# Kernel optimization log

Measured on AMD Instinct MI355X. Metric: run time of the kernel, lower is better.

Reference implementation:

```python
import jax, jax.numpy as jnp
import numpy as np
from jax import lax

B, T, D, H, O, L = 128, 2048, 64, 128, 32, 2


def _rnn_layer(x, lengths, W_ih, W_hh, b_ih, b_hh):
    """One tanh RNN layer over padded [B,T,*] input with packed semantics:
    hidden state is frozen at steps t >= lengths[b] (those steps do not exist
    in the packed sequence). Returns per-step hidden states [B,T,H]."""
    Bl, Tl, _ = x.shape
    Hl = W_hh.shape[0]
    # precompute input projection once: [B,T,H]
    x_proj = jnp.einsum('btd,hd->bth', x, W_ih) + b_ih + b_hh

    def step(h, inp):
        xp, t = inp  # xp: [B,H], t: scalar
        h_new = jnp.tanh(xp + h @ W_hh.T)
        h = jnp.where((t < lengths)[:, None], h_new, h)
        return h, h

    h0 = jnp.zeros((Bl, Hl), dtype=x.dtype)
    _, ys = lax.scan(step, h0, (x_proj.transpose(1, 0, 2), jnp.arange(Tl)))
    return ys.transpose(1, 0, 2)  # [B,T,H]


def setup_inputs() -> dict:
    key = jax.random.key(0)
    ks = jax.random.split(key, 12)
    x = jax.random.normal(ks[0], (B, T, D), dtype=jnp.float32)
    # descending-sorted lengths in [1, T] (pack_padded_sequence enforce_sorted)
    lengths = jnp.sort(jax.random.randint(ks[1], (B,), 1, T + 1).astype(jnp.int32))[::-1]
    s_in = 1.0 / np.sqrt(H)
    W_ih0 = jax.random.uniform(ks[2], (H, D), minval=-s_in, maxval=s_in)
    W_hh0 = jax.random.uniform(ks[3], (H, H), minval=-s_in, maxval=s_in)
    b_ih0 = jax.random.uniform(ks[4], (H,), minval=-s_in, maxval=s_in)
    b_hh0 = jax.random.uniform(ks[5], (H,), minval=-s_in, maxval=s_in)
    W_ih1 = jax.random.uniform(ks[6], (H, H), minval=-s_in, maxval=s_in)
    W_hh1 = jax.random.uniform(ks[7], (H, H), minval=-s_in, maxval=s_in)
    b_ih1 = jax.random.uniform(ks[8], (H,), minval=-s_in, maxval=s_in)
    b_hh1 = jax.random.uniform(ks[9], (H,), minval=-s_in, maxval=s_in)
    W_fc = jax.random.uniform(ks[10], (O, H), minval=-s_in, maxval=s_in)
    b_fc = jax.random.uniform(ks[11], (O,), minval=-s_in, maxval=s_in)
    return {"x": x, "lengths": lengths,
            "W_ih0": W_ih0, "W_hh0": W_hh0, "b_ih0": b_ih0, "b_hh0": b_hh0,
            "W_ih1": W_ih1, "W_hh1": W_hh1, "b_ih1": b_ih1, "b_hh1": b_hh1,
            "W_fc": W_fc, "b_fc": b_fc}


def reference(x, lengths, W_ih0, W_hh0, b_ih0, b_hh0,
              W_ih1, W_hh1, b_ih1, b_hh1, W_fc, b_fc):
    h1 = _rnn_layer(x, lengths, W_ih0, W_hh0, b_ih0, b_hh0)   # [B,T,H]
    h2 = _rnn_layer(h1, lengths, W_ih1, W_hh1, b_ih1, b_hh1)  # [B,T,H]
    # pad_packed_sequence zero-fills positions t >= length
    mask = (jnp.arange(T)[None, :] < lengths[:, None])[..., None]
    out = jnp.where(mask, h2, 0.0)
    # fc is applied to the zero-padded tensor (padded rows become b_fc)
    return jnp.einsum('bth,oh->bto', out, W_fc) + b_fc
```

## Files before the change

kernel.cpp:

```cpp
#include <hip/hip_runtime.h>

#define BB 128
#define TT 2048
#define DD 64
#define HH 128
#define OO 32

typedef _Float16 f16x8 __attribute__((ext_vector_type(8)));
typedef float    f32x4 __attribute__((ext_vector_type(4)));

#define MFMA16(a,b,c) __builtin_amdgcn_mfma_f32_16x16x32_f16((a),(b),(c),0,0,0)

__device__ __forceinline__ f32x4 load4(const float* p){ return *(const f32x4*)p; }

__device__ __forceinline__ f16x8 afrag(const float* p){
    float4 a = *(const float4*)p, b = *(const float4*)(p+4);
    f16x8 r;
    r[0]=(_Float16)a.x; r[1]=(_Float16)a.y; r[2]=(_Float16)a.z; r[3]=(_Float16)a.w;
    r[4]=(_Float16)b.x; r[5]=(_Float16)b.y; r[6]=(_Float16)b.z; r[7]=(_Float16)b.w;
    return r;
}

__device__ __forceinline__ float tanh5(float u){
#if __has_builtin(__builtin_amdgcn_exp2f)
    float e = __builtin_amdgcn_exp2f(u * 2.885390081777927f);
#else
    float e = exp2f(u * 2.885390081777927f);
#endif
    return __builtin_fmaf(-2.f, __builtin_amdgcn_rcpf(1.f + e), 1.f);
}

#define XSTR 72
extern "C" __global__ void __launch_bounds__(256)
proj_kernel(const float* __restrict__ x, const float* __restrict__ W_ih0,
            const float* __restrict__ b_ih0, const float* __restrict__ b_hh0,
            _Float16* __restrict__ xp0)
{
    const int tid = threadIdx.x;
    const int w = tid >> 6, lane = tid & 63;
    const int n = lane & 15, q = lane >> 4;
    const size_t row0 = (size_t)blockIdx.x * 64;

    __shared__ __align__(16) _Float16 XT[64][XSTR];

    #pragma unroll
    for (int it = 0; it < 4; ++it){
        float4 v = *(const float4*)(x + row0*DD + it*1024 + tid*4);
        int rr = it*16 + (tid >> 4), d0 = (tid & 15)*4;
        union { uint2 u; _Float16 h[4]; } c;
        c.h[0]=(_Float16)v.x; c.h[1]=(_Float16)v.y; c.h[2]=(_Float16)v.z; c.h[3]=(_Float16)v.w;
        *(uint2*)&XT[rr][d0] = c.u;
    }

    f16x8 A[8][2]; f32x4 bv[8];
    #pragma unroll
    for (int mt = 0; mt < 8; ++mt){
        #pragma unroll
        for (int kt = 0; kt < 2; ++kt)
            A[mt][kt] = afrag(W_ih0 + (mt*16 + n)*DD + kt*32 + q*8);
        bv[mt] = load4(b_ih0 + mt*16 + q*4) + load4(b_hh0 + mt*16 + q*4);
    }
    __syncthreads();

    const _Float16* xr = &XT[w*16 + n][0];
    f16x8 B0 = *(const f16x8*)(xr + q*8);
    f16x8 B1 = *(const f16x8*)(xr + 32 + q*8);

    _Float16* orow = xp0 + (row0 + w*16 + n)*HH + q*4;
    #pragma unroll
    for (int mt = 0; mt < 8; ++mt){
        f32x4 acc = bv[mt];
        acc = MFMA16(A[mt][0], B0, acc);
        acc = MFMA16(A[mt][1], B1, acc);
        union { uint2 u; _Float16 h[4]; } s;
        #pragma unroll
        for (int r = 0; r < 4; ++r) s.h[r] = (_Float16)acc[r];
        *(uint2*)(orow + mt*16) = s.u;
    }
}

extern "C" __global__ void __launch_bounds__(256)
fill_kernel(const int* __restrict__ lengths, const float* __restrict__ b_fc,
            float* __restrict__ out)
{
    size_t idx = (size_t)blockIdx.x*256 + threadIdx.x;
    #pragma unroll
    for (int k = 0; k < 4; ++k, idx += (size_t)2048*256){
        int o4 = (int)(idx & 7);
        int t  = (int)((idx >> 3) & 2047);
        int b  = (int)(idx >> 14);
        if (t >= lengths[b])
            ((float4*)out)[idx] = *(const float4*)(b_fc + o4*4);
    }
}

#define NB   16
#define LSTR 136

extern "C" __global__ void __launch_bounds__(256, 1)
scan_kernel(const _Float16* __restrict__ xp0, const int* __restrict__ lengths,
            const float* __restrict__ W_hh0,
            const float* __restrict__ W_ih1, const float* __restrict__ W_hh1,
            const float* __restrict__ b_ih1, const float* __restrict__ b_hh1,
            const float* __restrict__ W_fc,  const float* __restrict__ b_fc,
            float* __restrict__ out)
{
    const int tid  = threadIdx.x;
    const int w    = tid >> 6, lane = tid & 63;
    const int n    = lane & 15, q = lane >> 4;
    const int rbase= blockIdx.x * NB;

    __shared__ __align__(16) _Float16 H1T[2][NB][LSTR];
    __shared__ __align__(16) _Float16 H2T[2][NB][LSTR];

    for (int idx = tid; idx < 2*NB*LSTR/2; idx += 256){
        ((unsigned*)H1T)[idx] = 0u;
        ((unsigned*)H2T)[idx] = 0u;
    }

    f16x8 A0[2][4], Ai[2][4], Ah[2][4];
    #pragma unroll
    for (int m = 0; m < 2; ++m){
        const int row = (2*w + m)*16 + n;
        #pragma unroll
        for (int kt = 0; kt < 4; ++kt){
            A0[m][kt] = afrag(W_hh0 + row*HH + kt*32 + q*8);
            Ai[m][kt] = afrag(W_ih1 + row*HH + kt*32 + q*8);
            Ah[m][kt] = afrag(W_hh1 + row*HH + kt*32 + q*8);
        }
    }
    const int f = w & 1;
    f16x8 Af[4];
    #pragma unroll
    for (int kt = 0; kt < 4; ++kt)
        Af[kt] = afrag(W_fc + (f*16 + n)*HH + kt*32 + q*8);

    f32x4 b1v[2];
    #pragma unroll
    for (int m = 0; m < 2; ++m)
        b1v[m] = load4(b_ih1 + (2*w+m)*16 + q*4) + load4(b_hh1 + (2*w+m)*16 + q*4);
    const f32x4 bfv = load4(b_fc + f*16 + q*4);

    const int lenn = lengths[rbase + n];
    int mx = lenn;
    #pragma unroll
    for (int s = 1; s < 16; s <<= 1){ int o = __shfl_xor(mx, s, 64); mx = max(mx, o); }
    const int maxlen = __builtin_amdgcn_readfirstlane(mx);

    const _Float16* xpbase = xp0 + ((size_t)(rbase+n)*TT)*HH + (2*w)*16 + q*4;
    float* obase = out + ((size_t)(rbase+n)*TT)*OO + f*16 + q*4;

    uint2 xcA, xcB, xnA, xnB;
    xcA = *(const uint2*)(xpbase);            xcB = *(const uint2*)(xpbase + 16);
    if (1 < maxlen){ xnA = *(const uint2*)(xpbase + HH); xnB = *(const uint2*)(xpbase + HH + 16); }

    __syncthreads();

    for (int t = 0; t <= maxlen + 1; ++t){
        const int p = t & 1, pn = p ^ 1;

        f16x8 bh1[4], bh2[4];
        #pragma unroll
        for (int kt = 0; kt < 4; ++kt){
            bh1[kt] = *(const f16x8*)&H1T[p][n][kt*32 + q*8];
            bh2[kt] = *(const f16x8*)&H2T[p][n][kt*32 + q*8];
        }

        f32x4 z0[2];
        const bool doZ0 = (t < maxlen);
        if (doZ0){
            {
                union { uint2 u; _Float16 h[4]; } cA, cB; cA.u = xcA; cB.u = xcB;
                #pragma unroll
                for (int r = 0; r < 4; ++r){ z0[0][r] = (float)cA.h[r]; z0[1][r] = (float)cB.h[r]; }
            }
            if (t + 2 < maxlen){
                xcA = *(const uint2*)(xpbase + (size_t)(t+2)*HH);
                xcB = *(const uint2*)(xpbase + (size_t)(t+2)*HH + 16);
            }
            #pragma unroll
            for (int kt = 0; kt < 4; ++kt){
                z0[0] = MFMA16(A0[0][kt], bh1[kt], z0[0]);
                z0[1] = MFMA16(A0[1][kt], bh1[kt], z0[1]);
            }
        }

        f32x4 z1[2];
        const bool doZ1 = (t >= 1) && (t <= maxlen);
        if (doZ1){
            z1[0] = b1v[0]; z1[1] = b1v[1];
            #pragma unroll
            for (int kt = 0; kt < 4; ++kt){
                z1[0] = MFMA16(Ai[0][kt], bh1[kt], z1[0]);
                z1[1] = MFMA16(Ai[1][kt], bh1[kt], z1[1]);
            }
            #pragma unroll
            for (int kt = 0; kt < 4; ++kt){
                z1[0] = MFMA16(Ah[0][kt], bh2[kt], z1[0]);
                z1[1] = MFMA16(Ah[1][kt], bh2[kt], z1[1]);
            }
        }

        if (w >= 2 && t >= 2){
            f32x4 zf = bfv;
            #pragma unroll
            for (int kt = 0; kt < 4; ++kt) zf = MFMA16(Af[kt], bh2[kt], zf);
            if (t - 2 < lenn){
                float4 sv; sv.x = zf[0]; sv.y = zf[1]; sv.z = zf[2]; sv.w = zf[3];
                *(float4*)(obase + (size_t)(t-2)*OO) = sv;
            }
        }

        if (doZ0){
            #pragma unroll
            for (int m = 0; m < 2; ++m){
                union { uint2 u; _Float16 h[4]; } s;
                #pragma unroll
                for (int r = 0; r < 4; ++r) s.h[r] = (_Float16)tanh5(z0[m][r]);
                *(uint2*)&H1T[pn][n][(2*w+m)*16 + q*4] = s.u;
            }
        }
        if (doZ1){
            #pragma unroll
            for (int m = 0; m < 2; ++m){
                union { uint2 u; _Float16 h[4]; } s;
                #pragma unroll
                for (int r = 0; r < 4; ++r) s.h[r] = (_Float16)tanh5(z1[m][r]);
                *(uint2*)&H2T[pn][n][(2*w+m)*16 + q*4] = s.u;
            }
        }

        { uint2 tA = xcA; xcA = xnA; xnA = tA; uint2 tB = xcB; xcB = xnB; xnB = tB; }

        asm volatile("s_waitcnt lgkmcnt(0)\n\ts_barrier" ::: "memory");
    }
}

extern "C" void kernel_launch(void* const* d_in, const int* in_sizes, int n_in,
                              void* d_out, int out_size, void* d_ws, size_t ws_size,
                              hipStream_t stream)
{
    const float* x       = (const float*)d_in[0];
    const int*   lengths = (const int*)  d_in[1];
    const float* W_ih0   = (const float*)d_in[2];
    const float* W_hh0   = (const float*)d_in[3];
    const float* b_ih0   = (const float*)d_in[4];
    const float* b_hh0   = (const float*)d_in[5];
    const float* W_ih1   = (const float*)d_in[6];
    const float* W_hh1   = (const float*)d_in[7];
    const float* b_ih1   = (const float*)d_in[8];
    const float* b_hh1   = (const float*)d_in[9];
    const float* W_fc    = (const float*)d_in[10];
    const float* b_fc    = (const float*)d_in[11];

    _Float16* xp = (_Float16*)d_ws;

    proj_kernel<<<BB*TT/64, 256, 0, stream>>>(x, W_ih0, b_ih0, b_hh0, xp);
    fill_kernel<<<2048, 256, 0, stream>>>(lengths, b_fc, (float*)d_out);
    scan_kernel<<<BB/NB, 256, 0, stream>>>(xp, lengths, W_hh0,
                                           W_ih1, W_hh1, b_ih1, b_hh1,
                                           W_fc, b_fc, (float*)d_out);
}
```

Measured before the change: 1.783 ms.

## Pack two batch groups per workgroup with per-group LDS counter barriers

The scan kernel now launches 4 workgroups of 512 threads instead of 8 of 256. Each workgroup holds two independent 16-row batch groups, each with its own LDS state buffers. The per-step s_barrier is replaced by a per-group LDS atomic counter with a spin-wait, so the two groups synchronise independently. The intent is to cut barrier cost and let the two groups' waves interleave on one CU. In exchange it uses fewer CUs, adds atomic and spin-polling overhead, and doubles per-thread register pressure demands under the 512,2 launch bounds, which may force spills of the weight fragments.

```diff
diff --git a/kernel.cpp b/kernel.cpp
--- a/kernel.cpp
+++ b/kernel.cpp
@@ -97,7 +97,7 @@
 #define NB   16
 #define LSTR 136
 
-extern "C" __global__ void __launch_bounds__(256, 1)
+extern "C" __global__ void __launch_bounds__(512, 2)
 scan_kernel(const _Float16* __restrict__ xp0, const int* __restrict__ lengths,
             const float* __restrict__ W_hh0,
             const float* __restrict__ W_ih1, const float* __restrict__ W_hh1,
@@ -106,17 +106,23 @@
             float* __restrict__ out)
 {
     const int tid  = threadIdx.x;
-    const int w    = tid >> 6, lane = tid & 63;
+    const int grp  = tid >> 8;
+    const int wtid = tid & 255;
+    const int w    = wtid >> 6, lane = wtid & 63;
     const int n    = lane & 15, q = lane >> 4;
-    const int rbase= blockIdx.x * NB;
-
-    __shared__ __align__(16) _Float16 H1T[2][NB][LSTR];
-    __shared__ __align__(16) _Float16 H2T[2][NB][LSTR];
-
-    for (int idx = tid; idx < 2*NB*LSTR/2; idx += 256){
-        ((unsigned*)H1T)[idx] = 0u;
-        ((unsigned*)H2T)[idx] = 0u;
-    }
+    const int rbase= blockIdx.x * 32 + grp * NB;
+
+    __shared__ __align__(16) _Float16 H1T[2][2][NB][LSTR];
+    __shared__ __align__(16) _Float16 H2T[2][2][NB][LSTR];
+    __shared__ unsigned ctr[2];
+
+    for (int idx = wtid; idx < NB*LSTR/2; idx += 256){
+        ((unsigned*)&H1T[0][grp][0][0])[idx] = 0u;
+        ((unsigned*)&H1T[1][grp][0][0])[idx] = 0u;
+        ((unsigned*)&H2T[0][grp][0][0])[idx] = 0u;
+        ((unsigned*)&H2T[1][grp][0][0])[idx] = 0u;
+    }
+    if (tid < 2) ctr[tid] = 0u;
 
     f16x8 A0[2][4], Ai[2][4], Ah[2][4];
     #pragma unroll
@@ -156,14 +162,15 @@
 
     __syncthreads();
 
+    unsigned tgt = 4u;
     for (int t = 0; t <= maxlen + 1; ++t){
         const int p = t & 1, pn = p ^ 1;
 
         f16x8 bh1[4], bh2[4];
         #pragma unroll
         for (int kt = 0; kt < 4; ++kt){
-            bh1[kt] = *(const f16x8*)&H1T[p][n][kt*32 + q*8];
-            bh2[kt] = *(const f16x8*)&H2T[p][n][kt*32 + q*8];
+            bh1[kt] = *(const f16x8*)&H1T[p][grp][n][kt*32 + q*8];
+            bh2[kt] = *(const f16x8*)&H2T[p][grp][n][kt*32 + q*8];
         }
 
         f32x4 z0[2];
@@ -217,7 +224,7 @@
                 union { uint2 u; _Float16 h[4]; } s;
                 #pragma unroll
                 for (int r = 0; r < 4; ++r) s.h[r] = (_Float16)tanh5(z0[m][r]);
-                *(uint2*)&H1T[pn][n][(2*w+m)*16 + q*4] = s.u;
+                *(uint2*)&H1T[pn][grp][n][(2*w+m)*16 + q*4] = s.u;
             }
         }
         if (doZ1){
@@ -226,13 +233,20 @@
                 union { uint2 u; _Float16 h[4]; } s;
                 #pragma unroll
                 for (int r = 0; r < 4; ++r) s.h[r] = (_Float16)tanh5(z1[m][r]);
-                *(uint2*)&H2T[pn][n][(2*w+m)*16 + q*4] = s.u;
+                *(uint2*)&H2T[pn][grp][n][(2*w+m)*16 + q*4] = s.u;
             }
         }
 
         { uint2 tA = xcA; xcA = xnA; xnA = tA; uint2 tB = xcB; xcB = xnB; xnB = tB; }
 
-        asm volatile("s_waitcnt lgkmcnt(0)\n\ts_barrier" ::: "memory");
+        asm volatile("s_waitcnt lgkmcnt(0)" ::: "memory");
+        if (lane == 0)
+            __hip_atomic_fetch_add(&ctr[grp], 1u, __ATOMIC_RELEASE,
+                                   __HIP_MEMORY_SCOPE_WORKGROUP);
+        while (__hip_atomic_load(&ctr[grp], __ATOMIC_ACQUIRE,
+                                 __HIP_MEMORY_SCOPE_WORKGROUP) < tgt)
+            __builtin_amdgcn_s_sleep(1);
+        tgt += 4u;
     }
 }
 
@@ -257,7 +271,7 @@
 
     proj_kernel<<<BB*TT/64, 256, 0, stream>>>(x, W_ih0, b_ih0, b_hh0, xp);
     fill_kernel<<<2048, 256, 0, stream>>>(lengths, b_fc, (float*)d_out);
-    scan_kernel<<<BB/NB, 256, 0, stream>>>(xp, lengths, W_hh0,
+    scan_kernel<<<BB/32, 512, 0, stream>>>(xp, lengths, W_hh0,
                                            W_ih1, W_hh1, b_ih1, b_hh1,
                                            W_fc, b_fc, (float*)d_out);
 }
```

Result: slower. 2.059 ms (+15.5%).

## Split scan into warp-specialized pipeline stages with LDS flag handshakes

Applied to the files above, without the earlier changes.

The lockstep scan, where every wave did a slice of every stage and hit a block barrier each step, becomes a producer/consumer pipeline. Wave 0 runs the layer-0 recurrence, wave 1 the layer-1 input projection, wave 2 the layer-1 recurrence, and wave 3 the FC output. They pass data through 4-deep ring buffers in LDS using acquire/release flags. The tanh scale factor is folded into the weights and biases, and packed conversion plus swizzled LDS layouts are used. The layer-1 input projection now runs off the critical recurrence path. The cost is that each recurrence wave must issue all 32 MFMAs serially, and spin-waiting adds latency.

```diff
diff --git a/kernel.cpp b/kernel.cpp
--- a/kernel.cpp
+++ b/kernel.cpp
@@ -5,29 +5,71 @@
 #define DD 64
 #define HH 128
 #define OO 32
+#define NB 16
+#define SCALE 2.885390081777927f
 
 typedef _Float16 f16x8 __attribute__((ext_vector_type(8)));
+typedef __fp16   pk16x2 __attribute__((ext_vector_type(2)));
 typedef float    f32x4 __attribute__((ext_vector_type(4)));
 
 #define MFMA16(a,b,c) __builtin_amdgcn_mfma_f32_16x16x32_f16((a),(b),(c),0,0,0)
 
 __device__ __forceinline__ f32x4 load4(const float* p){ return *(const f32x4*)p; }
 
-__device__ __forceinline__ f16x8 afrag(const float* p){
+__device__ __forceinline__ f16x8 afrag_s(const float* p, float s){
     float4 a = *(const float4*)p, b = *(const float4*)(p+4);
     f16x8 r;
-    r[0]=(_Float16)a.x; r[1]=(_Float16)a.y; r[2]=(_Float16)a.z; r[3]=(_Float16)a.w;
-    r[4]=(_Float16)b.x; r[5]=(_Float16)b.y; r[6]=(_Float16)b.z; r[7]=(_Float16)b.w;
+    r[0]=(_Float16)(a.x*s); r[1]=(_Float16)(a.y*s); r[2]=(_Float16)(a.z*s); r[3]=(_Float16)(a.w*s);
+    r[4]=(_Float16)(b.x*s); r[5]=(_Float16)(b.y*s); r[6]=(_Float16)(b.z*s); r[7]=(_Float16)(b.w*s);
     return r;
 }
 
-__device__ __forceinline__ float tanh5(float u){
+__device__ __forceinline__ float tanh_pre(float z){
 #if __has_builtin(__builtin_amdgcn_exp2f)
-    float e = __builtin_amdgcn_exp2f(u * 2.885390081777927f);
+    float e = __builtin_amdgcn_exp2f(z);
 #else
-    float e = exp2f(u * 2.885390081777927f);
+    float e = exp2f(z);
 #endif
     return __builtin_fmaf(-2.f, __builtin_amdgcn_rcpf(1.f + e), 1.f);
+}
+
+__device__ __forceinline__ unsigned pk2(float a, float b){
+    union { pk16x2 h; unsigned u; } c;
+    c.h = __builtin_amdgcn_cvt_pkrtz(a, b);
+    return c.u;
+}
+
+__device__ __forceinline__ unsigned ld_flag(const unsigned* p){
+    return __hip_atomic_load(p, __ATOMIC_ACQUIRE, __HIP_MEMORY_SCOPE_WORKGROUP);
+}
+__device__ __forceinline__ void st_flag(unsigned* p, unsigned v){
+    __hip_atomic_store(p, v, __ATOMIC_RELEASE, __HIP_MEMORY_SCOPE_WORKGROUP);
+}
+
+__device__ __forceinline__ void read_frags(const unsigned* slot, int n, int q, int swz,
+                                           f16x8* f){
+    #pragma unroll
+    for (int kt = 0; kt < 4; ++kt){
+        const int c4 = (kt*4 + q) ^ swz;
+        f[kt] = *(const f16x8*)&slot[n*64 + c4*4];
+    }
+}
+__device__ __forceinline__ void write_pack(unsigned* slot, int n, int q, int swz,
+                                           const unsigned P[8][2]){
+    #pragma unroll
+    for (int mt = 0; mt < 8; ++mt){
+        const int c4 = (mt*2 + (q>>1)) ^ swz;
+        uint2 v; v.x = P[mt][0]; v.y = P[mt][1];
+        *(uint2*)&slot[n*64 + c4*4 + (q&1)*2] = v;
+    }
+}
+__device__ __forceinline__ void tanh_pack(const f32x4* z, unsigned P[8][2]){
+    #pragma unroll
+    for (int mt = 0; mt < 8; ++mt){
+        float t0 = tanh_pre(z[mt][0]), t1 = tanh_pre(z[mt][1]);
+        float t2 = tanh_pre(z[mt][2]), t3 = tanh_pre(z[mt][3]);
+        P[mt][0] = pk2(t0, t1); P[mt][1] = pk2(t2, t3);
+    }
 }
 
 #define XSTR 72
@@ -57,8 +99,8 @@
     for (int mt = 0; mt < 8; ++mt){
         #pragma unroll
         for (int kt = 0; kt < 2; ++kt)
-            A[mt][kt] = afrag(W_ih0 + (mt*16 + n)*DD + kt*32 + q*8);
-        bv[mt] = load4(b_ih0 + mt*16 + q*4) + load4(b_hh0 + mt*16 + q*4);
+            A[mt][kt] = afrag_s(W_ih0 + (mt*16 + n)*DD + kt*32 + q*8, SCALE);
+        bv[mt] = (load4(b_ih0 + mt*16 + q*4) + load4(b_hh0 + mt*16 + q*4)) * SCALE;
     }
     __syncthreads();
 
@@ -94,52 +136,26 @@
     }
 }
 
-#define NB   16
-#define LSTR 136
-
 extern "C" __global__ void __launch_bounds__(256, 1)
-scan_kernel(const _Float16* __restrict__ xp0, const int* __restrict__ lengths,
-            const float* __restrict__ W_hh0,
-            const float* __restrict__ W_ih1, const float* __restrict__ W_hh1,
-            const float* __restrict__ b_ih1, const float* __restrict__ b_hh1,
-            const float* __restrict__ W_fc,  const float* __restrict__ b_fc,
-            float* __restrict__ out)
+scan_pipe(const _Float16* __restrict__ xp0, const int* __restrict__ lengths,
+          const float* __restrict__ W_hh0,
+          const float* __restrict__ W_ih1, const float* __restrict__ W_hh1,
+          const float* __restrict__ b_ih1, const float* __restrict__ b_hh1,
+          const float* __restrict__ W_fc,  const float* __restrict__ b_fc,
+          float* __restrict__ out)
 {
     const int tid  = threadIdx.x;
     const int w    = tid >> 6, lane = tid & 63;
     const int n    = lane & 15, q = lane >> 4;
-    const int rbase= blockIdx.x * NB;
-
-    __shared__ __align__(16) _Float16 H1T[2][NB][LSTR];
-    __shared__ __align__(16) _Float16 H2T[2][NB][LSTR];
-
-    for (int idx = tid; idx < 2*NB*LSTR/2; idx += 256){
-        ((unsigned*)H1T)[idx] = 0u;
-        ((unsigned*)H2T)[idx] = 0u;
-    }
-
-    f16x8 A0[2][4], Ai[2][4], Ah[2][4];
-    #pragma unroll
-    for (int m = 0; m < 2; ++m){
-        const int row = (2*w + m)*16 + n;
-        #pragma unroll
-        for (int kt = 0; kt < 4; ++kt){
-            A0[m][kt] = afrag(W_hh0 + row*HH + kt*32 + q*8);
-            Ai[m][kt] = afrag(W_ih1 + row*HH + kt*32 + q*8);
-            Ah[m][kt] = afrag(W_hh1 + row*HH + kt*32 + q*8);
-        }
-    }
-    const int f = w & 1;
-    f16x8 Af[4];
-    #pragma unroll
-    for (int kt = 0; kt < 4; ++kt)
-        Af[kt] = afrag(W_fc + (f*16 + n)*HH + kt*32 + q*8);
-
-    f32x4 b1v[2];
-    #pragma unroll
-    for (int m = 0; m < 2; ++m)
-        b1v[m] = load4(b_ih1 + (2*w+m)*16 + q*4) + load4(b_hh1 + (2*w+m)*16 + q*4);
-    const f32x4 bfv = load4(b_fc + f*16 + q*4);
+    const int swz  = (n >> 1) & 7;
+    const int rbase = blockIdx.x * NB;
+
+    __shared__ __align__(16) unsigned h1slot[4][NB*64];
+    __shared__ __align__(16) unsigned h2slot[4][NB*64];
+    __shared__ __align__(16) f32x4    uslot[4][64*8];
+    __shared__ unsigned flg[8];
+
+    if (tid < 8) flg[tid] = 0u;
 
     const int lenn = lengths[rbase + n];
     int mx = lenn;
@@ -147,92 +163,162 @@
     for (int s = 1; s < 16; s <<= 1){ int o = __shfl_xor(mx, s, 64); mx = max(mx, o); }
     const int maxlen = __builtin_amdgcn_readfirstlane(mx);
 
-    const _Float16* xpbase = xp0 + ((size_t)(rbase+n)*TT)*HH + (2*w)*16 + q*4;
-    float* obase = out + ((size_t)(rbase+n)*TT)*OO + f*16 + q*4;
-
-    uint2 xcA, xcB, xnA, xnB;
-    xcA = *(const uint2*)(xpbase);            xcB = *(const uint2*)(xpbase + 16);
-    if (1 < maxlen){ xnA = *(const uint2*)(xpbase + HH); xnB = *(const uint2*)(xpbase + HH + 16); }
-
     __syncthreads();
 
-    for (int t = 0; t <= maxlen + 1; ++t){
-        const int p = t & 1, pn = p ^ 1;
-
-        f16x8 bh1[4], bh2[4];
-        #pragma unroll
-        for (int kt = 0; kt < 4; ++kt){
-            bh1[kt] = *(const f16x8*)&H1T[p][n][kt*32 + q*8];
-            bh2[kt] = *(const f16x8*)&H2T[p][n][kt*32 + q*8];
-        }
-
-        f32x4 z0[2];
-        const bool doZ0 = (t < maxlen);
-        if (doZ0){
-            {
-                union { uint2 u; _Float16 h[4]; } cA, cB; cA.u = xcA; cB.u = xcB;
+    if (w == 0){
+        f16x8 A0[8][4];
+        #pragma unroll
+        for (int mt = 0; mt < 8; ++mt)
+            #pragma unroll
+            for (int kt = 0; kt < 4; ++kt)
+                A0[mt][kt] = afrag_s(W_hh0 + (mt*16 + n)*HH + kt*32 + q*8, SCALE);
+
+        const _Float16* xpb = xp0 + (size_t)(rbase + n)*TT*HH + q*4;
+        uint2 xc[8], xn[8];
+        #pragma unroll
+        for (int mt = 0; mt < 8; ++mt) xc[mt] = *(const uint2*)(xpb + mt*16);
+        #pragma unroll
+        for (int mt = 0; mt < 8; ++mt)
+            xn[mt] = (1 < maxlen) ? *(const uint2*)(xpb + HH + mt*16) : xc[mt];
+
+        f16x8 bh1[4];
+        #pragma unroll
+        for (int kt = 0; kt < 4; ++kt) bh1[kt] = (f16x8)(_Float16)0;
+
+        unsigned cons = 0;
+        for (int t = 0; t < maxlen; ++t){
+            if (t >= 4 && cons < (unsigned)(t-3)){
+                do { cons = ld_flag(&flg[1]); } while (cons < (unsigned)(t-3));
+            }
+            f32x4 z[8];
+            #pragma unroll
+            for (int mt = 0; mt < 8; ++mt){
+                union { uint2 u; _Float16 h[4]; } c; c.u = xc[mt];
+                z[mt][0]=(float)c.h[0]; z[mt][1]=(float)c.h[1];
+                z[mt][2]=(float)c.h[2]; z[mt][3]=(float)c.h[3];
+            }
+            if (t + 2 < maxlen){
                 #pragma unroll
-                for (int r = 0; r < 4; ++r){ z0[0][r] = (float)cA.h[r]; z0[1][r] = (float)cB.h[r]; }
-            }
-            if (t + 2 < maxlen){
-                xcA = *(const uint2*)(xpbase + (size_t)(t+2)*HH);
-                xcB = *(const uint2*)(xpbase + (size_t)(t+2)*HH + 16);
-            }
+                for (int mt = 0; mt < 8; ++mt)
+                    xc[mt] = *(const uint2*)(xpb + (size_t)(t+2)*HH + mt*16);
+            }
+            #pragma unroll
+            for (int kt = 0; kt < 4; ++kt)
+                #pragma unroll
+                for (int mt = 0; mt < 8; ++mt)
+                    z[mt] = MFMA16(A0[mt][kt], bh1[kt], z[mt]);
+
+            unsigned P[8][2];
+            tanh_pack(z, P);
+            unsigned* slot = h1slot[t & 3];
+            write_pack(slot, n, q, swz, P);
+            read_frags(slot, n, q, swz, bh1);
+            if (lane == 0) st_flag(&flg[0], (unsigned)(t+1));
+
+            #pragma unroll
+            for (int mt = 0; mt < 8; ++mt){ uint2 tmp = xc[mt]; xc[mt] = xn[mt]; xn[mt] = tmp; }
+        }
+    } else if (w == 1){
+        f16x8 Ai[8][4]; f32x4 b1v[8];
+        #pragma unroll
+        for (int mt = 0; mt < 8; ++mt){
+            #pragma unroll
+            for (int kt = 0; kt < 4; ++kt)
+                Ai[mt][kt] = afrag_s(W_ih1 + (mt*16 + n)*HH + kt*32 + q*8, SCALE);
+            b1v[mt] = (load4(b_ih1 + mt*16 + q*4) + load4(b_hh1 + mt*16 + q*4)) * SCALE;
+        }
+        unsigned prod = 0, cons = 0;
+        const int l7 = lane & 7;
+        for (int t = 0; t < maxlen; ++t){
+            if (prod <= (unsigned)t){
+                do { prod = ld_flag(&flg[0]); } while (prod <= (unsigned)t);
+            }
+            f16x8 bh1[4];
+            read_frags(h1slot[t & 3], n, q, swz, bh1);
+            if (t >= 4 && cons < (unsigned)(t-3)){
+                do { cons = ld_flag(&flg[3]); } while (cons < (unsigned)(t-3));
+            }
+            f32x4 u[8];
+            #pragma unroll
+            for (int mt = 0; mt < 8; ++mt) u[mt] = b1v[mt];
+            #pragma unroll
+            for (int kt = 0; kt < 4; ++kt)
+                #pragma unroll
+                for (int mt = 0; mt < 8; ++mt)
+                    u[mt] = MFMA16(Ai[mt][kt], bh1[kt], u[mt]);
+            f32x4* us = uslot[t & 3];
+            #pragma unroll
+            for (int mt = 0; mt < 8; ++mt) us[lane*8 + (mt ^ l7)] = u[mt];
+            if (lane == 0){ st_flag(&flg[1], (unsigned)(t+1)); st_flag(&flg[2], (unsigned)(t+1)); }
+        }
+    } else if (w == 2){
+        f16x8 Ah[8][4];
+        #pragma unroll
+        for (int mt = 0; mt < 8; ++mt)
+            #pragma unroll
+            for (int kt = 0; kt < 4; ++kt)
+                Ah[mt][kt] = afrag_s(W_hh1 + (mt*16 + n)*HH + kt*32 + q*8, SCALE);
+        f16x8 bh2[4];
+        #pragma unroll
+        for (int kt = 0; kt < 4; ++kt) bh2[kt] = (f16x8)(_Float16)0;
+
+        unsigned prod = 0, cons = 0;
+        const int l7 = lane & 7;
+        for (int t = 0; t < maxlen; ++t){
+            if (prod <= (unsigned)t){
+                do { prod = ld_flag(&flg[2]); } while (prod <= (unsigned)t);
+            }
+            if (t >= 4 && cons < (unsigned)(t-3)){
+                do { cons = ld_flag(&flg[5]); } while (cons < (unsigned)(t-3));
+            }
+            f32x4 z[8];
+            const f32x4* us = uslot[t & 3];
+            #pragma unroll
+            for (int mt = 0; mt < 8; ++mt) z[mt] = us[lane*8 + (mt ^ l7)];
+            #pragma unroll
+            for (int kt = 0; kt < 4; ++kt)
+                #pragma unroll
+                for (int mt = 0; mt < 8; ++mt)
+                    z[mt] = MFMA16(Ah[mt][kt], bh2[kt], z[mt]);
+
+            unsigned P[8][2];
+            tanh_pack(z, P);
+            unsigned* slot = h2slot[t & 3];
+            write_pack(slot, n, q, swz, P);
+            read_frags(slot, n, q, swz, bh2);
+            if (lane == 0){ st_flag(&flg[3], (unsigned)(t+1)); st_flag(&flg[4], (unsigned)(t+1)); }
+        }
+    } else {
+        f16x8 Af[2][4]; f32x4 bfv[2];
+        #pragma unroll
+        for (int mt = 0; mt < 2; ++mt){
+            #pragma unroll
+            for (int kt = 0; kt < 4; ++kt)
+                Af[mt][kt] = afrag_s(W_fc + (mt*16 + n)*HH + kt*32 + q*8, 1.0f);
+            bfv[mt] = load4(b_fc + mt*16 + q*4);
+        }
+        float* ob = out + (size_t)(rbase + n)*TT*OO + q*4;
+        unsigned prod = 0;
+        for (int t = 0; t < maxlen; ++t){
+            if (prod <= (unsigned)t){
+                do { prod = ld_flag(&flg[4]); } while (prod <= (unsigned)t);
+            }
+            f16x8 bh2[4];
+            read_frags(h2slot[t & 3], n, q, swz, bh2);
+            f32x4 zf0 = bfv[0], zf1 = bfv[1];
             #pragma unroll
             for (int kt = 0; kt < 4; ++kt){
-                z0[0] = MFMA16(A0[0][kt], bh1[kt], z0[0]);
-                z0[1] = MFMA16(A0[1][kt], bh1[kt], z0[1]);
-            }
-        }
-
-        f32x4 z1[2];
-        const bool doZ1 = (t >= 1) && (t <= maxlen);
-        if (doZ1){
-            z1[0] = b1v[0]; z1[1] = b1v[1];
-            #pragma unroll
-            for (int kt = 0; kt < 4; ++kt){
-                z1[0] = MFMA16(Ai[0][kt], bh1[kt], z1[0]);
-                z1[1] = MFMA16(Ai[1][kt], bh1[kt], z1[1]);
-            }
-            #pragma unroll
-            for (int kt = 0; kt < 4; ++kt){
-                z1[0] = MFMA16(Ah[0][kt], bh2[kt], z1[0]);
-                z1[1] = MFMA16(Ah[1][kt], bh2[kt], z1[1]);
-            }
-        }
-
-        if (w >= 2 && t >= 2){
-            f32x4 zf = bfv;
-            #pragma unroll
-            for (int kt = 0; kt < 4; ++kt) zf = MFMA16(Af[kt], bh2[kt], zf);
-            if (t - 2 < lenn){
-                float4 sv; sv.x = zf[0]; sv.y = zf[1]; sv.z = zf[2]; sv.w = zf[3];
-                *(float4*)(obase + (size_t)(t-2)*OO) = sv;
-            }
-        }
-
-        if (doZ0){
-            #pragma unroll
-            for (int m = 0; m < 2; ++m){
-                union { uint2 u; _Float16 h[4]; } s;
-                #pragma unroll
-                for (int r = 0; r < 4; ++r) s.h[r] = (_Float16)tanh5(z0[m][r]);
-                *(uint2*)&H1T[pn][n][(2*w+m)*16 + q*4] = s.u;
-            }
-        }
-        if (doZ1){
-            #pragma unroll
-            for (int m = 0; m < 2; ++m){
-                union { uint2 u; _Float16 h[4]; } s;
-                #pragma unroll
-                for (int r = 0; r < 4; ++r) s.h[r] = (_Float16)tanh5(z1[m][r]);
-                *(uint2*)&H2T[pn][n][(2*w+m)*16 + q*4] = s.u;
-            }
-        }
-
-        { uint2 tA = xcA; xcA = xnA; xnA = tA; uint2 tB = xcB; xcB = xnB; xnB = tB; }
-
-        asm volatile("s_waitcnt lgkmcnt(0)\n\ts_barrier" ::: "memory");
+                zf0 = MFMA16(Af[0][kt], bh2[kt], zf0);
+                zf1 = MFMA16(Af[1][kt], bh2[kt], zf1);
+            }
+            if (lane == 0) st_flag(&flg[5], (unsigned)(t+1));
+            if (t < lenn){
+                float4 s0; s0.x=zf0[0]; s0.y=zf0[1]; s0.z=zf0[2]; s0.w=zf0[3];
+                float4 s1; s1.x=zf1[0]; s1.y=zf1[1]; s1.z=zf1[2]; s1.w=zf1[3];
+                *(float4*)(ob + (size_t)t*OO)      = s0;
+                *(float4*)(ob + (size_t)t*OO + 16) = s1;
+            }
+        }
     }
 }
 
@@ -257,7 +343,7 @@
 
     proj_kernel<<<BB*TT/64, 256, 0, stream>>>(x, W_ih0, b_ih0, b_hh0, xp);
     fill_kernel<<<2048, 256, 0, stream>>>(lengths, b_fc, (float*)d_out);
-    scan_kernel<<<BB/NB, 256, 0, stream>>>(xp, lengths, W_hh0,
-                                           W_ih1, W_hh1, b_ih1, b_hh1,
-                                           W_fc, b_fc, (float*)d_out);
-}
+    scan_pipe<<<BB/NB, 256, 0, stream>>>(xp, lengths, W_hh0,
+                                         W_ih1, W_hh1, b_ih1, b_hh1,
+                                         W_fc, b_fc, (float*)d_out);
+}
```

New measurement: 4.119 ms. 2.31x slower.
